# Kernel optimization log

Measured on AMD Instinct MI355X. Metric: run time of the kernel, lower is better.

The kernel has to match this reference:

```python
import jax, jax.numpy as jnp
import numpy as np

NEG_SLOPE = 0.01  # torch F.leaky_relu default
N_USER = 100000
N_ITEM = 100000
N_EDGE = 640000
D = 128
N_LAYERS = 3  # 1 input + num_hidden_layers(1) + 1 output layer


def setup_inputs() -> dict:
    key = jax.random.key(0)
    ks = jax.random.split(key, 10)
    scale = 1.0 / np.sqrt(D)
    return {
        "h_user": jax.random.normal(ks[0], (N_USER, D), dtype=jnp.float32),
        "h_item": jax.random.normal(ks[1], (N_ITEM, D), dtype=jnp.float32),
        # W[layer, etype] : etype 0 = user-follows->user, 1 = user-clicks->item, 2 = item-clicked_by->user
        "W": jax.random.normal(ks[2], (N_LAYERS, 3, D, D), dtype=jnp.float32) * scale,
        "b": jnp.zeros((N_LAYERS, 3, D), dtype=jnp.float32),
        "follows_src": jax.random.randint(ks[3], (N_EDGE,), 0, N_USER, dtype=jnp.int32),
        "follows_dst": jax.random.randint(ks[4], (N_EDGE,), 0, N_USER, dtype=jnp.int32),
        "clicks_src": jax.random.randint(ks[5], (N_EDGE,), 0, N_USER, dtype=jnp.int32),
        "clicks_dst": jax.random.randint(ks[6], (N_EDGE,), 0, N_ITEM, dtype=jnp.int32),
        "cb_src": jax.random.randint(ks[7], (N_EDGE,), 0, N_ITEM, dtype=jnp.int32),
        "cb_dst": jax.random.randint(ks[8], (N_EDGE,), 0, N_USER, dtype=jnp.int32),
    }


def _etype_conv(h_src, W, b, src, dst, n_dst):
    """Per-etype Linear on src nodes, copy_u gather, mean-aggregate at dst."""
    Wh = h_src @ W + b                     # [N_src, D] dense transform (once per node)
    msg = Wh[src]                          # [E, D] gather
    s = jax.ops.segment_sum(msg, dst, num_segments=n_dst)
    cnt = jax.ops.segment_sum(jnp.ones((src.shape[0],), dtype=Wh.dtype), dst, num_segments=n_dst)
    return s / jnp.maximum(cnt, 1.0)[:, None]  # mean; isolated nodes -> 0


def _rgcn_forward(h_user, h_item, W, b, follows_src, follows_dst,
                  clicks_src, clicks_dst, cb_src, cb_dst):
    hu, hi = h_user, h_item
    for l in range(N_LAYERS):
        # per-etype mean aggregation, then cross-etype 'sum' (DGL multi_update_all)
        agg_u = (_etype_conv(hu, W[l, 0], b[l, 0], follows_src, follows_dst, N_USER)
                 + _etype_conv(hi, W[l, 2], b[l, 2], cb_src, cb_dst, N_USER))
        agg_i = _etype_conv(hu, W[l, 1], b[l, 1], clicks_src, clicks_dst, N_ITEM)
        hu = jax.nn.leaky_relu(agg_u, NEG_SLOPE)
        hi = jax.nn.leaky_relu(agg_i, NEG_SLOPE)
    return jnp.stack([hu, hi])  # [2, 100000, 128]


def reference(h_user, h_item, W, b, follows_src, follows_dst,
              clicks_src, clicks_dst, cb_src, cb_dst):
    return _rgcn_forward(h_user, h_item, W, b, follows_src, follows_dst,
                         clicks_src, clicks_dst, cb_src, cb_dst)
```

## Files before the change

kernel.cpp:

```cpp
#include <hip/hip_runtime.h>

typedef unsigned short u16;
typedef _Float16 f16;
typedef __attribute__((ext_vector_type(2))) _Float16 f16x2;
typedef __attribute__((ext_vector_type(8))) _Float16 f16x8;
typedef __attribute__((ext_vector_type(2))) float f32x2;
typedef __attribute__((ext_vector_type(4))) float f32x4;

#define D 128

__global__ __launch_bounds__(256) void k_convert(const float* __restrict__ in,
                                                 u16* __restrict__ out, int n8) {
  int i = blockIdx.x * 256 + threadIdx.x;
  if (i >= n8) return;
  const float4* ip = (const float4*)in;
  float4 a = ip[i * 2], b = ip[i * 2 + 1];
  f16x8 v = {(f16)a.x, (f16)a.y, (f16)a.z, (f16)a.w,
             (f16)b.x, (f16)b.y, (f16)b.z, (f16)b.w};
  *(f16x8*)(out + (size_t)i * 8) = v;
}

__global__ __launch_bounds__(256) void k_convW(const float* __restrict__ W,
                                               u16* __restrict__ Wt, int total) {
  int idx = blockIdx.x * 256 + threadIdx.x;
  if (idx >= total) return;
  int mat = idx >> 14;
  int k = (idx >> 7) & 127;
  int n = idx & 127;
  f16 v = (f16)W[idx];
  ((f16*)Wt)[(size_t)mat * 16384 + n * 128 + k] = v;
}

__global__ __launch_bounds__(256) void k_count(const int* __restrict__ dst,
                                               int* __restrict__ cnt, int nE) {
  int e = blockIdx.x * 256 + threadIdx.x;
  if (e < nE) atomicAdd(&cnt[dst[e]], 1);
}

__global__ __launch_bounds__(256) void k_scanA(const int* __restrict__ cnt,
                                               int* __restrict__ part, int n) {
  int t = threadIdx.x;
  int idx = blockIdx.x * 1024 + t * 4;
  int4 v = {0, 0, 0, 0};
  if (idx + 3 < n)
    v = *(const int4*)(cnt + idx);
  else {
    if (idx < n) v.x = cnt[idx];
    if (idx + 1 < n) v.y = cnt[idx + 1];
    if (idx + 2 < n) v.z = cnt[idx + 2];
    if (idx + 3 < n) v.w = cnt[idx + 3];
  }
  int s = v.x + v.y + v.z + v.w;
  for (int off = 1; off < 64; off <<= 1) s += __shfl_down(s, off, 64);
  __shared__ int ws[4];
  if ((t & 63) == 0) ws[t >> 6] = s;
  __syncthreads();
  if (t == 0) part[blockIdx.x] = ws[0] + ws[1] + ws[2] + ws[3];
}

__global__ __launch_bounds__(1024) void k_scanB(int* __restrict__ part, int n_part) {
  __shared__ int sh[1024];
  int t = threadIdx.x;
  int v = (t < n_part) ? part[t] : 0;
  sh[t] = v;
  __syncthreads();
  for (int off = 1; off < 1024; off <<= 1) {
    int u = (t >= off) ? sh[t - off] : 0;
    __syncthreads();
    sh[t] += u;
    __syncthreads();
  }
  if (t < n_part) part[t] = sh[t] - v;
}

__global__ __launch_bounds__(256) void k_scanC(const int* __restrict__ cnt,
                                               const int* __restrict__ part,
                                               int* __restrict__ rs,
                                               int n, int total) {
  int t = threadIdx.x;
  int idx = blockIdx.x * 1024 + t * 4;
  int4 v = {0, 0, 0, 0};
  if (idx + 3 < n)
    v = *(const int4*)(cnt + idx);
  else {
    if (idx < n) v.x = cnt[idx];
    if (idx + 1 < n) v.y = cnt[idx + 1];
    if (idx + 2 < n) v.z = cnt[idx + 2];
    if (idx + 3 < n) v.w = cnt[idx + 3];
  }
  int s = v.x + v.y + v.z + v.w;
  int inc = s;
  int lane = t & 63, w = t >> 6;
  for (int off = 1; off < 64; off <<= 1) {
    int u = __shfl_up(inc, off, 64);
    if (lane >= off) inc += u;
  }
  __shared__ int ws[4];
  if (lane == 63) ws[w] = inc;
  __syncthreads();
  int woff = 0;
  for (int i = 0; i < w; ++i) woff += ws[i];
  int ex = part[blockIdx.x] + woff + inc - s;
  int4 r;
  r.x = ex;
  r.y = ex + v.x;
  r.z = r.y + v.y;
  r.w = r.z + v.z;
  if (idx + 3 < n)
    *(int4*)(rs + idx) = r;
  else {
    if (idx < n) rs[idx] = r.x;
    if (idx + 1 < n) rs[idx + 1] = r.y;
    if (idx + 2 < n) rs[idx + 2] = r.z;
    if (idx + 3 < n) rs[idx + 3] = r.w;
  }
  if (blockIdx.x == 0 && t == 0) rs[n] = total;
}

__global__ __launch_bounds__(256) void k_fill(const int* __restrict__ src,
                                              const int* __restrict__ dst,
                                              const int* __restrict__ rs,
                                              int* __restrict__ cnt,
                                              int* __restrict__ csr, int nE, int soff) {
  int e = blockIdx.x * 256 + threadIdx.x;
  if (e < nE) {
    int d = dst[e];
    int p = atomicSub(&cnt[d], 1);
    csr[rs[d] + p - 1] = src[e] + soff;
  }
}

__global__ __launch_bounds__(256) void k_agg3(
    const u16* __restrict__ h_all, const int* __restrict__ csr,
    const int* __restrict__ rs, u16* __restrict__ M_all, int N3) {
  int wave = (blockIdx.x * 256 + threadIdx.x) >> 6;
  int lane = threadIdx.x & 63;
  int l16 = lane & 15;
  int w = wave * 4 + (lane >> 4);
  bool valid = w < N3;
  int wc = valid ? w : 0;
  int e = rs[wc];
  int en = valid ? rs[wc + 1] : 0;
  int deg = en - e;
  f32x2 ac0 = {0.f, 0.f}, ac1 = {0.f, 0.f}, ac2 = {0.f, 0.f}, ac3 = {0.f, 0.f};
  const char* hb = (const char*)h_all;
  unsigned loff = (unsigned)l16 * 16u;

  while (__any(e < en)) {
    bool a0 = e < en, a1 = e + 1 < en;
    int s0 = 0, s1 = 0;
    if (a0) s0 = csr[e];
    if (a1) s1 = csr[e + 1];
    f16x8 v0 = {0, 0, 0, 0, 0, 0, 0, 0}, v1 = {0, 0, 0, 0, 0, 0, 0, 0};
    if (a0) v0 = *(const f16x8*)(hb + ((unsigned)s0 * 256u + loff));
    if (a1) v1 = *(const f16x8*)(hb + ((unsigned)s1 * 256u + loff));
    ac0 += (f32x2){(float)v0[0], (float)v0[1]};
    ac1 += (f32x2){(float)v0[2], (float)v0[3]};
    ac2 += (f32x2){(float)v0[4], (float)v0[5]};
    ac3 += (f32x2){(float)v0[6], (float)v0[7]};
    ac0 += (f32x2){(float)v1[0], (float)v1[1]};
    ac1 += (f32x2){(float)v1[2], (float)v1[3]};
    ac2 += (f32x2){(float)v1[4], (float)v1[5]};
    ac3 += (f32x2){(float)v1[6], (float)v1[7]};
    e += 2;
  }

  if (valid) {
    float inv = deg ? 1.0f / (float)deg : 0.f;
    f16x8 r = {(f16)(ac0[0] * inv), (f16)(ac0[1] * inv),
               (f16)(ac1[0] * inv), (f16)(ac1[1] * inv),
               (f16)(ac2[0] * inv), (f16)(ac2[1] * inv),
               (f16)(ac3[0] * inv), (f16)(ac3[1] * inv)};
    *(f16x8*)((char*)M_all + ((unsigned)wc * 256u + loff)) = r;
  }
}

template <int NE, int OUTF32>
__device__ __forceinline__ void gemm_body(
    f16 (*Wt)[128][136],
    const u16* __restrict__ mA, const u16* __restrict__ mBp,
    const u16* __restrict__ wtA, const u16* __restrict__ wtB,
    const float* __restrict__ bA, const float* __restrict__ bB,
    const int* __restrict__ rsA, const int* __restrict__ rsB,
    u16* __restrict__ o16, float* __restrict__ o32, int M, int blk) {
  int tid = threadIdx.x;
  {
    const f16x8* wa = (const f16x8*)wtA;
    for (int idx = tid; idx < 128 * 16; idx += 256) {
      int n = idx >> 4, c = idx & 15;
      *(f16x8*)&Wt[0][n][c * 8] = wa[idx];
    }
    if (NE == 2) {
      const f16x8* wb = (const f16x8*)wtB;
      for (int idx = tid; idx < 128 * 16; idx += 256) {
        int n = idx >> 4, c = idx & 15;
        *(f16x8*)&Wt[1][n][c * 8] = wb[idx];
      }
    }
  }
  __syncthreads();

  int lane = tid & 63, w = tid >> 6;
  int lr = lane & 15;
  int lk = (lane >> 4) * 8;
  long row0 = (long)blk * 128 + w * 32;

  f32x4 acc[2][8];
#pragma unroll
  for (int rt = 0; rt < 2; rt++)
#pragma unroll
    for (int n = 0; n < 8; n++) acc[rt][n] = (f32x4){0.f, 0.f, 0.f, 0.f};

#pragma unroll
  for (int e = 0; e < NE; ++e) {
    const f16* mm = (const f16*)((e == 0) ? mA : mBp);
#pragma unroll
    for (int ks = 0; ks < 4; ++ks) {
      int k0 = ks * 32 + lk;
      f16x8 bf[8];
#pragma unroll
      for (int n = 0; n < 8; n++) bf[n] = *(const f16x8*)&Wt[e][n * 16 + lr][k0];
#pragma unroll
      for (int rt = 0; rt < 2; rt++) {
        long r = row0 + rt * 16 + lr;
        if (r >= M) r = M - 1;
        f16x8 af = *(const f16x8*)(mm + r * D + k0);
#pragma unroll
        for (int n = 0; n < 8; n++)
          acc[rt][n] = __builtin_amdgcn_mfma_f32_16x16x32_f16(af, bf[n], acc[rt][n], 0, 0, 0);
      }
    }
  }

  float bAr[8], bBr[8];
#pragma unroll
  for (int n = 0; n < 8; n++) {
    bAr[n] = bA[n * 16 + lr];
    bBr[n] = (NE == 2) ? bB[n * 16 + lr] : 0.f;
  }

#pragma unroll
  for (int rt = 0; rt < 2; rt++) {
    long rbase = row0 + rt * 16 + (lane >> 4) * 4;
#pragma unroll
    for (int i = 0; i < 4; i++) {
      long r = rbase + i;
      if (r < M) {
        bool mAok = rsA[r + 1] > rsA[r];
        bool mBok = (NE == 2) && (rsB[r + 1] > rsB[r]);
#pragma unroll
        for (int n = 0; n < 8; n++) {
          int col = n * 16 + lr;
          float v = acc[rt][n][i];
          if (mAok) v += bAr[n];
          if (mBok) v += bBr[n];
          v = v > 0.f ? v : 0.01f * v;
          if (OUTF32)
            o32[r * D + col] = v;
          else
            ((f16*)o16)[r * D + col] = (f16)v;
        }
      }
    }
  }
}

template <int OUTF32>
__global__ __launch_bounds__(256) void k_gemm2(
    const u16* __restrict__ M_all, const u16* __restrict__ Wl,
    const float* __restrict__ bl, const int* __restrict__ rs_all,
    u16* __restrict__ h_all, float* __restrict__ out,
    int NU, int NI, int nbI) {
  __shared__ __align__(16) f16 Wt[2][128][136];
  if ((int)blockIdx.x < nbI) {
    gemm_body<1, OUTF32>(Wt,
                         M_all + (size_t)NU * D, nullptr,
                         Wl + 16384, nullptr,
                         bl + D, nullptr,
                         rs_all + NU, nullptr,
                         h_all + (size_t)NU * D, out + (size_t)NU * D, NI,
                         blockIdx.x);
  } else {
    gemm_body<2, OUTF32>(Wt,
                         M_all, M_all + (size_t)(NU + NI) * D,
                         Wl, Wl + 2 * 16384,
                         bl, bl + 2 * D,
                         rs_all, rs_all + NU + NI,
                         h_all, out, NU, blockIdx.x - nbI);
  }
}

extern "C" void kernel_launch(void* const* d_in, const int* in_sizes, int n_in,
                              void* d_out, int out_size, void* d_ws, size_t ws_size,
                              hipStream_t stream) {
  const float* h_user = (const float*)d_in[0];
  const float* h_item = (const float*)d_in[1];
  const float* W = (const float*)d_in[2];
  const float* bb = (const float*)d_in[3];
  const int* f_src = (const int*)d_in[4];
  const int* f_dst = (const int*)d_in[5];
  const int* c_src = (const int*)d_in[6];
  const int* c_dst = (const int*)d_in[7];
  const int* cb_src = (const int*)d_in[8];
  const int* cb_dst = (const int*)d_in[9];

  const int NU = in_sizes[0] / D;
  const int NI = in_sizes[1] / D;
  const int nEf = in_sizes[4], nEc = in_sizes[6], nEcb = in_sizes[8];
  const int N3 = NU + NI + NU;
  const int nE = nEf + nEc + nEcb;

  char* p = (char*)d_ws;
  auto alloc = [&](size_t bytes) {
    char* r = p;
    p += (bytes + 255) & ~(size_t)255;
    return r;
  };
  int* cnt_all = (int*)alloc((size_t)N3 * 4);
  int* rs_all = (int*)alloc((size_t)(N3 + 1) * 4);
  int* part = (int*)alloc(1024 * 4);
  u16* Wtg = (u16*)alloc((size_t)9 * 16384 * 2);
  int* csr_all = (int*)alloc((size_t)nE * 4);
  u16* h_all = (u16*)alloc((size_t)(NU + NI) * D * 2);
  u16* M_all = (u16*)alloc((size_t)N3 * D * 2);
  (void)ws_size;

  hipMemsetAsync(cnt_all, 0, (size_t)N3 * 4, stream);

  k_convert<<<(NU * D / 8 + 255) / 256, 256, 0, stream>>>(h_user, h_all, NU * D / 8);
  k_convert<<<(NI * D / 8 + 255) / 256, 256, 0, stream>>>(h_item, h_all + (size_t)NU * D,
                                                          NI * D / 8);
  k_convW<<<(9 * 16384 + 255) / 256, 256, 0, stream>>>(W, Wtg, 9 * 16384);

  k_count<<<(nEf + 255) / 256, 256, 0, stream>>>(f_dst, cnt_all, nEf);
  k_count<<<(nEc + 255) / 256, 256, 0, stream>>>(c_dst, cnt_all + NU, nEc);
  k_count<<<(nEcb + 255) / 256, 256, 0, stream>>>(cb_dst, cnt_all + NU + NI, nEcb);

  int n_part = (N3 + 1023) / 1024;
  k_scanA<<<n_part, 256, 0, stream>>>(cnt_all, part, N3);
  k_scanB<<<1, 1024, 0, stream>>>(part, n_part);
  k_scanC<<<n_part, 256, 0, stream>>>(cnt_all, part, rs_all, N3, nE);

  k_fill<<<(nEf + 255) / 256, 256, 0, stream>>>(f_src, f_dst, rs_all, cnt_all,
                                                csr_all, nEf, 0);
  k_fill<<<(nEc + 255) / 256, 256, 0, stream>>>(c_src, c_dst, rs_all + NU, cnt_all + NU,
                                                csr_all, nEc, 0);
  k_fill<<<(nEcb + 255) / 256, 256, 0, stream>>>(cb_src, cb_dst, rs_all + NU + NI,
                                                 cnt_all + NU + NI, csr_all, nEcb, NU);

  int nbI = (NI + 127) / 128;
  int nbU = (NU + 127) / 128;
  int agg_blocks = ((N3 + 3) / 4 + 3) / 4;

  for (int l = 0; l < 3; ++l) {
    const u16* Wl = Wtg + (size_t)l * 3 * 16384;
    const float* bl = bb + (size_t)l * 3 * D;

    k_agg3<<<agg_blocks, 256, 0, stream>>>(h_all, csr_all, rs_all, M_all, N3);

    if (l < 2)
      k_gemm2<0><<<nbI + nbU, 256, 0, stream>>>(M_all, Wl, bl, rs_all, h_all,
                                                (float*)d_out, NU, NI, nbI);
    else
      k_gemm2<1><<<nbI + nbU, 256, 0, stream>>>(M_all, Wl, bl, rs_all, h_all,
                                                (float*)d_out, NU, NI, nbI);
  }
}
```

Baseline: 586.6 us.

## Fuse neighbor aggregation into GEMM via LDS staging, merge count/fill launches

Each layer's gather-mean aggregation now runs inside the GEMM kernel: a block gathers its 128 destination rows into shared memory, then runs MFMA against W read directly from global (no longer staged in LDS). The intermediate M buffer write and read are removed, and h is double-buffered (ping-pong) so the in-place overwrite hazard is avoided. The three per-etype count and fill kernels are also merged into single launches. The trade-off is that the gather and the MFMA phases are serialized within a block, and the user blocks do two gather/MFMA passes, which may cut latency hiding and occupancy.

Measured after the change: 1.043 ms. 1.78x slower.

```diff
diff --git a/kernel.cpp b/kernel.cpp
--- a/kernel.cpp
+++ b/kernel.cpp
@@ -2,12 +2,12 @@
 
 typedef unsigned short u16;
 typedef _Float16 f16;
-typedef __attribute__((ext_vector_type(2))) _Float16 f16x2;
 typedef __attribute__((ext_vector_type(8))) _Float16 f16x8;
 typedef __attribute__((ext_vector_type(2))) float f32x2;
 typedef __attribute__((ext_vector_type(4))) float f32x4;
 
 #define D 128
+#define LDW 136
 
 __global__ __launch_bounds__(256) void k_convert(const float* __restrict__ in,
                                                  u16* __restrict__ out, int n8) {
@@ -31,10 +31,17 @@
   ((f16*)Wt)[(size_t)mat * 16384 + n * 128 + k] = v;
 }
 
-__global__ __launch_bounds__(256) void k_count(const int* __restrict__ dst,
-                                               int* __restrict__ cnt, int nE) {
+__global__ __launch_bounds__(256) void k_count3(
+    const int* __restrict__ fd, const int* __restrict__ cd,
+    const int* __restrict__ cbd, int* __restrict__ cnt,
+    int NU, int NI, int nf, int nc, int ncb) {
   int e = blockIdx.x * 256 + threadIdx.x;
-  if (e < nE) atomicAdd(&cnt[dst[e]], 1);
+  if (e < nf)
+    atomicAdd(&cnt[fd[e]], 1);
+  else if (e < nf + nc)
+    atomicAdd(&cnt[NU + cd[e - nf]], 1);
+  else if (e < nf + nc + ncb)
+    atomicAdd(&cnt[NU + NI + cbd[e - nf - nc]], 1);
 }
 
 __global__ __launch_bounds__(256) void k_scanA(const int* __restrict__ cnt,
@@ -117,148 +124,128 @@
   if (blockIdx.x == 0 && t == 0) rs[n] = total;
 }
 
-__global__ __launch_bounds__(256) void k_fill(const int* __restrict__ src,
-                                              const int* __restrict__ dst,
-                                              const int* __restrict__ rs,
-                                              int* __restrict__ cnt,
-                                              int* __restrict__ csr, int nE, int soff) {
+__global__ __launch_bounds__(256) void k_fill3(
+    const int* __restrict__ fs, const int* __restrict__ fd,
+    const int* __restrict__ cs, const int* __restrict__ cd,
+    const int* __restrict__ cbs, const int* __restrict__ cbd,
+    const int* __restrict__ rs, int* __restrict__ cnt, int* __restrict__ csr,
+    int NU, int NI, int nf, int nc, int ncb) {
   int e = blockIdx.x * 256 + threadIdx.x;
-  if (e < nE) {
-    int d = dst[e];
-    int p = atomicSub(&cnt[d], 1);
-    csr[rs[d] + p - 1] = src[e] + soff;
-  }
-}
-
-__global__ __launch_bounds__(256) void k_agg3(
+  int d, s;
+  if (e < nf) {
+    d = fd[e];
+    s = fs[e];
+  } else if (e < nf + nc) {
+    d = NU + cd[e - nf];
+    s = cs[e - nf];
+  } else if (e < nf + nc + ncb) {
+    d = NU + NI + cbd[e - nf - nc];
+    s = cbs[e - nf - nc] + NU;
+  } else
+    return;
+  int p = atomicSub(&cnt[d], 1);
+  csr[rs[d] + p - 1] = s;
+}
+
+__device__ __forceinline__ void gather_lds(f16 (*Msh)[LDW],
     const u16* __restrict__ h_all, const int* __restrict__ csr,
-    const int* __restrict__ rs, u16* __restrict__ M_all, int N3) {
-  int wave = (blockIdx.x * 256 + threadIdx.x) >> 6;
-  int lane = threadIdx.x & 63;
-  int l16 = lane & 15;
-  int w = wave * 4 + (lane >> 4);
-  bool valid = w < N3;
-  int wc = valid ? w : 0;
-  int e = rs[wc];
-  int en = valid ? rs[wc + 1] : 0;
-  int deg = en - e;
-  f32x2 ac0 = {0.f, 0.f}, ac1 = {0.f, 0.f}, ac2 = {0.f, 0.f}, ac3 = {0.f, 0.f};
+    const int* __restrict__ rs_all, int gbase, int Mrows) {
+  int tid = threadIdx.x;
+  int wv = tid >> 6, lane = tid & 63, l16 = lane & 15, grp = lane >> 4;
   const char* hb = (const char*)h_all;
   unsigned loff = (unsigned)l16 * 16u;
-
-  while (__any(e < en)) {
-    bool a0 = e < en, a1 = e + 1 < en;
-    int s0 = 0, s1 = 0;
-    if (a0) s0 = csr[e];
-    if (a1) s1 = csr[e + 1];
-    f16x8 v0 = {0, 0, 0, 0, 0, 0, 0, 0}, v1 = {0, 0, 0, 0, 0, 0, 0, 0};
-    if (a0) v0 = *(const f16x8*)(hb + ((unsigned)s0 * 256u + loff));
-    if (a1) v1 = *(const f16x8*)(hb + ((unsigned)s1 * 256u + loff));
-    ac0 += (f32x2){(float)v0[0], (float)v0[1]};
-    ac1 += (f32x2){(float)v0[2], (float)v0[3]};
-    ac2 += (f32x2){(float)v0[4], (float)v0[5]};
-    ac3 += (f32x2){(float)v0[6], (float)v0[7]};
-    ac0 += (f32x2){(float)v1[0], (float)v1[1]};
-    ac1 += (f32x2){(float)v1[2], (float)v1[3]};
-    ac2 += (f32x2){(float)v1[4], (float)v1[5]};
-    ac3 += (f32x2){(float)v1[6], (float)v1[7]};
-    e += 2;
-  }
-
-  if (valid) {
-    float inv = deg ? 1.0f / (float)deg : 0.f;
-    f16x8 r = {(f16)(ac0[0] * inv), (f16)(ac0[1] * inv),
-               (f16)(ac1[0] * inv), (f16)(ac1[1] * inv),
-               (f16)(ac2[0] * inv), (f16)(ac2[1] * inv),
-               (f16)(ac3[0] * inv), (f16)(ac3[1] * inv)};
-    *(f16x8*)((char*)M_all + ((unsigned)wc * 256u + loff)) = r;
+#pragma unroll 1
+  for (int it = 0; it < 8; ++it) {
+    int nidx = wv * 32 + it * 4 + grp;
+    bool valid = nidx < Mrows;
+    int g = gbase + (valid ? nidx : 0);
+    int e = rs_all[g];
+    int en = valid ? rs_all[g + 1] : e;
+    int deg = en - e;
+    f32x2 ac0 = {0.f, 0.f}, ac1 = {0.f, 0.f}, ac2 = {0.f, 0.f}, ac3 = {0.f, 0.f};
+    while (__any(e < en)) {
+      bool a0 = e < en, a1 = e + 1 < en;
+      int s0 = a0 ? csr[e] : 0;
+      int s1 = a1 ? csr[e + 1] : 0;
+      f16x8 v0 = {0, 0, 0, 0, 0, 0, 0, 0}, v1 = {0, 0, 0, 0, 0, 0, 0, 0};
+      if (a0) v0 = *(const f16x8*)(hb + ((unsigned)s0 * 256u + loff));
+      if (a1) v1 = *(const f16x8*)(hb + ((unsigned)s1 * 256u + loff));
+      ac0 += (f32x2){(float)v0[0], (float)v0[1]};
+      ac1 += (f32x2){(float)v0[2], (float)v0[3]};
+      ac2 += (f32x2){(float)v0[4], (float)v0[5]};
+      ac3 += (f32x2){(float)v0[6], (float)v0[7]};
+      ac0 += (f32x2){(float)v1[0], (float)v1[1]};
+      ac1 += (f32x2){(float)v1[2], (float)v1[3]};
+      ac2 += (f32x2){(float)v1[4], (float)v1[5]};
+      ac3 += (f32x2){(float)v1[6], (float)v1[7]};
+      e += 2;
+    }
+    if (valid) {
+      float inv = deg > 0 ? 1.0f / (float)deg : 0.f;
+      f16x8 r = {(f16)(ac0[0] * inv), (f16)(ac0[1] * inv),
+                 (f16)(ac1[0] * inv), (f16)(ac1[1] * inv),
+                 (f16)(ac2[0] * inv), (f16)(ac2[1] * inv),
+                 (f16)(ac3[0] * inv), (f16)(ac3[1] * inv)};
+      *(f16x8*)&Msh[nidx][l16 * 8] = r;
+    }
+  }
+}
+
+__device__ __forceinline__ void mfma_pass(f32x4 acc[2][8],
+    const f16 (*Msh)[LDW], const u16* __restrict__ Wmat) {
+  int tid = threadIdx.x, lane = tid & 63, wv = tid >> 6;
+  int lr = lane & 15, lk = (lane >> 4) * 8;
+  const f16* Wg = (const f16*)Wmat;
+#pragma unroll
+  for (int ks = 0; ks < 4; ++ks) {
+    int k0 = ks * 32 + lk;
+    f16x8 bf[8];
+#pragma unroll
+    for (int n = 0; n < 8; ++n)
+      bf[n] = *(const f16x8*)(Wg + (n * 16 + lr) * D + k0);
+#pragma unroll
+    for (int rt = 0; rt < 2; ++rt) {
+      f16x8 af = *(const f16x8*)&Msh[wv * 32 + rt * 16 + lr][k0];
+#pragma unroll
+      for (int n = 0; n < 8; ++n)
+        acc[rt][n] = __builtin_amdgcn_mfma_f32_16x16x32_f16(af, bf[n], acc[rt][n], 0, 0, 0);
+    }
   }
 }
 
 template <int NE, int OUTF32>
-__device__ __forceinline__ void gemm_body(
-    f16 (*Wt)[128][136],
-    const u16* __restrict__ mA, const u16* __restrict__ mBp,
-    const u16* __restrict__ wtA, const u16* __restrict__ wtB,
+__device__ __forceinline__ void epilogue(f32x4 acc[2][8],
     const float* __restrict__ bA, const float* __restrict__ bB,
     const int* __restrict__ rsA, const int* __restrict__ rsB,
-    u16* __restrict__ o16, float* __restrict__ o32, int M, int blk) {
-  int tid = threadIdx.x;
-  {
-    const f16x8* wa = (const f16x8*)wtA;
-    for (int idx = tid; idx < 128 * 16; idx += 256) {
-      int n = idx >> 4, c = idx & 15;
-      *(f16x8*)&Wt[0][n][c * 8] = wa[idx];
-    }
-    if (NE == 2) {
-      const f16x8* wb = (const f16x8*)wtB;
-      for (int idx = tid; idx < 128 * 16; idx += 256) {
-        int n = idx >> 4, c = idx & 15;
-        *(f16x8*)&Wt[1][n][c * 8] = wb[idx];
-      }
-    }
-  }
-  __syncthreads();
-
-  int lane = tid & 63, w = tid >> 6;
+    u16* __restrict__ o16, float* __restrict__ o32, int Mrows) {
+  int tid = threadIdx.x, lane = tid & 63, wv = tid >> 6;
   int lr = lane & 15;
-  int lk = (lane >> 4) * 8;
-  long row0 = (long)blk * 128 + w * 32;
-
-  f32x4 acc[2][8];
-#pragma unroll
-  for (int rt = 0; rt < 2; rt++)
-#pragma unroll
-    for (int n = 0; n < 8; n++) acc[rt][n] = (f32x4){0.f, 0.f, 0.f, 0.f};
-
-#pragma unroll
-  for (int e = 0; e < NE; ++e) {
-    const f16* mm = (const f16*)((e == 0) ? mA : mBp);
-#pragma unroll
-    for (int ks = 0; ks < 4; ++ks) {
-      int k0 = ks * 32 + lk;
-      f16x8 bf[8];
-#pragma unroll
-      for (int n = 0; n < 8; n++) bf[n] = *(const f16x8*)&Wt[e][n * 16 + lr][k0];
-#pragma unroll
-      for (int rt = 0; rt < 2; rt++) {
-        long r = row0 + rt * 16 + lr;
-        if (r >= M) r = M - 1;
-        f16x8 af = *(const f16x8*)(mm + r * D + k0);
-#pragma unroll
-        for (int n = 0; n < 8; n++)
-          acc[rt][n] = __builtin_amdgcn_mfma_f32_16x16x32_f16(af, bf[n], acc[rt][n], 0, 0, 0);
-      }
-    }
-  }
-
   float bAr[8], bBr[8];
 #pragma unroll
-  for (int n = 0; n < 8; n++) {
+  for (int n = 0; n < 8; ++n) {
     bAr[n] = bA[n * 16 + lr];
     bBr[n] = (NE == 2) ? bB[n * 16 + lr] : 0.f;
   }
-
-#pragma unroll
-  for (int rt = 0; rt < 2; rt++) {
-    long rbase = row0 + rt * 16 + (lane >> 4) * 4;
-#pragma unroll
-    for (int i = 0; i < 4; i++) {
-      long r = rbase + i;
-      if (r < M) {
+#pragma unroll
+  for (int rt = 0; rt < 2; ++rt) {
+    int rbase = wv * 32 + rt * 16 + (lane >> 4) * 4;
+#pragma unroll
+    for (int i = 0; i < 4; ++i) {
+      int r = rbase + i;
+      if (r < Mrows) {
         bool mAok = rsA[r + 1] > rsA[r];
-        bool mBok = (NE == 2) && (rsB[r + 1] > rsB[r]);
-#pragma unroll
-        for (int n = 0; n < 8; n++) {
+        bool mBok = (NE == 2) && rsB[r + 1] > rsB[r];
+#pragma unroll
+        for (int n = 0; n < 8; ++n) {
           int col = n * 16 + lr;
           float v = acc[rt][n][i];
           if (mAok) v += bAr[n];
           if (mBok) v += bBr[n];
           v = v > 0.f ? v : 0.01f * v;
           if (OUTF32)
-            o32[r * D + col] = v;
+            o32[(size_t)r * D + col] = v;
           else
-            ((f16*)o16)[r * D + col] = (f16)v;
+            ((f16*)o16)[(size_t)r * D + col] = (f16)v;
         }
       }
     }
@@ -266,27 +253,39 @@
 }
 
 template <int OUTF32>
-__global__ __launch_bounds__(256) void k_gemm2(
-    const u16* __restrict__ M_all, const u16* __restrict__ Wl,
-    const float* __restrict__ bl, const int* __restrict__ rs_all,
-    u16* __restrict__ h_all, float* __restrict__ out,
-    int NU, int NI, int nbI) {
-  __shared__ __align__(16) f16 Wt[2][128][136];
+__global__ __launch_bounds__(256) void k_fused(
+    const u16* __restrict__ hcur, const int* __restrict__ csr,
+    const int* __restrict__ rs_all, const u16* __restrict__ Wl,
+    const float* __restrict__ bl, u16* __restrict__ hnxt,
+    float* __restrict__ out, int NU, int NI, int nbI) {
+  __shared__ __align__(16) f16 Msh[128][LDW];
+  f32x4 acc[2][8];
+#pragma unroll
+  for (int rt = 0; rt < 2; ++rt)
+#pragma unroll
+    for (int n = 0; n < 8; ++n) acc[rt][n] = (f32x4){0.f, 0.f, 0.f, 0.f};
+
   if ((int)blockIdx.x < nbI) {
-    gemm_body<1, OUTF32>(Wt,
-                         M_all + (size_t)NU * D, nullptr,
-                         Wl + 16384, nullptr,
-                         bl + D, nullptr,
-                         rs_all + NU, nullptr,
-                         h_all + (size_t)NU * D, out + (size_t)NU * D, NI,
-                         blockIdx.x);
+    int m0 = blockIdx.x * 128;
+    int Mr = min(128, NI - m0);
+    gather_lds(Msh, hcur, csr, rs_all, NU + m0, Mr);
+    __syncthreads();
+    mfma_pass(acc, Msh, Wl + 16384);
+    epilogue<1, OUTF32>(acc, bl + D, nullptr, rs_all + NU + m0, nullptr,
+                        hnxt + (size_t)(NU + m0) * D,
+                        out + (size_t)(NU + m0) * D, Mr);
   } else {
-    gemm_body<2, OUTF32>(Wt,
-                         M_all, M_all + (size_t)(NU + NI) * D,
-                         Wl, Wl + 2 * 16384,
-                         bl, bl + 2 * D,
-                         rs_all, rs_all + NU + NI,
-                         h_all, out, NU, blockIdx.x - nbI);
+    int m0 = (blockIdx.x - nbI) * 128;
+    int Mr = min(128, NU - m0);
+    gather_lds(Msh, hcur, csr, rs_all, m0, Mr);
+    __syncthreads();
+    mfma_pass(acc, Msh, Wl);
+    __syncthreads();
+    gather_lds(Msh, hcur, csr, rs_all, NU + NI + m0, Mr);
+    __syncthreads();
+    mfma_pass(acc, Msh, Wl + 2 * 16384);
+    epilogue<2, OUTF32>(acc, bl, bl + 2 * D, rs_all + m0, rs_all + NU + NI + m0,
+                        hnxt + (size_t)m0 * D, out + (size_t)m0 * D, Mr);
   }
 }
 
@@ -321,48 +320,45 @@
   int* part = (int*)alloc(1024 * 4);
   u16* Wtg = (u16*)alloc((size_t)9 * 16384 * 2);
   int* csr_all = (int*)alloc((size_t)nE * 4);
-  u16* h_all = (u16*)alloc((size_t)(NU + NI) * D * 2);
-  u16* M_all = (u16*)alloc((size_t)N3 * D * 2);
+  u16* hA = (u16*)alloc((size_t)(NU + NI) * D * 2);
+  u16* hB = (u16*)alloc((size_t)(NU + NI) * D * 2);
   (void)ws_size;
 
   hipMemsetAsync(cnt_all, 0, (size_t)N3 * 4, stream);
 
-  k_convert<<<(NU * D / 8 + 255) / 256, 256, 0, stream>>>(h_user, h_all, NU * D / 8);
-  k_convert<<<(NI * D / 8 + 255) / 256, 256, 0, stream>>>(h_item, h_all + (size_t)NU * D,
+  k_convert<<<(NU * D / 8 + 255) / 256, 256, 0, stream>>>(h_user, hA, NU * D / 8);
+  k_convert<<<(NI * D / 8 + 255) / 256, 256, 0, stream>>>(h_item, hA + (size_t)NU * D,
                                                           NI * D / 8);
   k_convW<<<(9 * 16384 + 255) / 256, 256, 0, stream>>>(W, Wtg, 9 * 16384);
 
-  k_count<<<(nEf + 255) / 256, 256, 0, stream>>>(f_dst, cnt_all, nEf);
-  k_count<<<(nEc + 255) / 256, 256, 0, stream>>>(c_dst, cnt_all + NU, nEc);
-  k_count<<<(nEcb + 255) / 256, 256, 0, stream>>>(cb_dst, cnt_all + NU + NI, nEcb);
+  k_count3<<<(nE + 255) / 256, 256, 0, stream>>>(f_dst, c_dst, cb_dst, cnt_all,
+                                                 NU, NI, nEf, nEc, nEcb);
 
   int n_part = (N3 + 1023) / 1024;
   k_scanA<<<n_part, 256, 0, stream>>>(cnt_all, part, N3);
   k_scanB<<<1, 1024, 0, stream>>>(part, n_part);
   k_scanC<<<n_part, 256, 0, stream>>>(cnt_all, part, rs_all, N3, nE);
 
-  k_fill<<<(nEf + 255) / 256, 256, 0, stream>>>(f_src, f_dst, rs_all, cnt_all,
-                                                csr_all, nEf, 0);
-  k_fill<<<(nEc + 255) / 256, 256, 0, stream>>>(c_src, c_dst, rs_all + NU, cnt_all + NU,
-                                                csr_all, nEc, 0);
-  k_fill<<<(nEcb + 255) / 256, 256, 0, stream>>>(cb_src, cb_dst, rs_all + NU + NI,
-                                                 cnt_all + NU + NI, csr_all, nEcb, NU);
+  k_fill3<<<(nE + 255) / 256, 256, 0, stream>>>(f_src, f_dst, c_src, c_dst,
+                                                cb_src, cb_dst, rs_all, cnt_all,
+                                                csr_all, NU, NI, nEf, nEc, nEcb);
 
   int nbI = (NI + 127) / 128;
   int nbU = (NU + 127) / 128;
-  int agg_blocks = ((N3 + 3) / 4 + 3) / 4;
-
+
+  u16* hcur = hA;
+  u16* hnxt = hB;
   for (int l = 0; l < 3; ++l) {
     const u16* Wl = Wtg + (size_t)l * 3 * 16384;
     const float* bl = bb + (size_t)l * 3 * D;
-
-    k_agg3<<<agg_blocks, 256, 0, stream>>>(h_all, csr_all, rs_all, M_all, N3);
-
     if (l < 2)
-      k_gemm2<0><<<nbI + nbU, 256, 0, stream>>>(M_all, Wl, bl, rs_all, h_all,
-                                                (float*)d_out, NU, NI, nbI);
+      k_fused<0><<<nbI + nbU, 256, 0, stream>>>(hcur, csr_all, rs_all, Wl, bl,
+                                                hnxt, (float*)d_out, NU, NI, nbI);
     else
-      k_gemm2<1><<<nbI + nbU, 256, 0, stream>>>(M_all, Wl, bl, rs_all, h_all,
-                                                (float*)d_out, NU, NI, nbI);
-  }
-}
+      k_fused<1><<<nbI + nbU, 256, 0, stream>>>(hcur, csr_all, rs_all, Wl, bl,
+                                                hnxt, (float*)d_out, NU, NI, nbI);
+    u16* t = hcur;
+    hcur = hnxt;
+    hnxt = t;
+  }
+}
```
